# Performance work log

Hardware: AMD Instinct MI355X
Metric: run time of the kernel (lower is better)

The kernel has to match this reference:

```python
import jax, jax.numpy as jnp
import numpy as np

SCORE_WEIGHT = 0.5
MAX_ITER = 20
PROJ_ITER = 5
RELAX_LR = 0.1
EPS = 1e-8

P, D, T, O, H, W = 256, 256, 2, 24, 240, 432


def setup_inputs() -> dict:
    key = jax.random.key(0)
    k1, k2, k3, k4, k5 = jax.random.split(key, 5)
    proposed_feature = jax.random.normal(k1, (P, D), dtype=jnp.float32)
    proposed_mask = (jax.random.uniform(k2, (P, H, W)) > 0.7).astype(jnp.float32)
    template_feature = jax.random.normal(k3, (T, O, D), dtype=jnp.float32)
    mask_last_occurence = (jax.random.uniform(k4, (O, H, W)) > 0.7).astype(jnp.float32)
    proposal_score = jax.random.uniform(k5, (P,), dtype=jnp.float32)
    return {
        "proposed_feature": proposed_feature,
        "proposed_mask": proposed_mask,
        "template_feature": template_feature,
        "mask_last_occurence": mask_last_occurence,
        "proposal_score": proposal_score,
    }


def relax_matching(C, max_iter=MAX_ITER, proj_iter=PROJ_INNER if False else PROJ_ITER, lr=RELAX_LR):
    """Projected-gradient relaxation of the assignment LP.
    Gradient step on <C, X>, then proj_iter alternating projections onto
    {X >= 0, X <= 1, row sums == 1}. Returns mean of iterates (sum(X_list)/len)."""
    K, N = C.shape
    X0 = jnp.full((K, N), 1.0 / N, dtype=C.dtype)

    def project(X):
        def body(_, X):
            X = jnp.clip(X, 0.0, 1.0)
            X = X / (jnp.sum(X, axis=1, keepdims=True) + EPS)
            return X
        return jax.lax.fori_loop(0, proj_iter, body, X)

    def step(X, _):
        X = project(X - lr * C)
        return X, X

    _, Xs = jax.lax.scan(step, X0, None, length=max_iter)
    return jnp.mean(Xs, axis=0)  # [K, N]


def reference(proposed_feature, proposed_mask, template_feature,
              mask_last_occurence, proposal_score):
    n_prop = proposed_mask.shape[0]
    n_tplt = mask_last_occurence.shape[0]
    h, w = proposed_mask.shape[1], proposed_mask.shape[2]

    # --- feature cosine similarity, averaged over template frames ---
    kf = proposed_feature / (jnp.linalg.norm(proposed_feature, axis=1, keepdims=True) + EPS)
    qf = template_feature / (jnp.linalg.norm(template_feature, axis=2, keepdims=True) + EPS)
    feature_sim = jnp.einsum('tod,pd->op', qf, kf) / template_feature.shape[0]  # [O, P]

    # --- pairwise binary-mask IoU without materializing [O*P, HW] ---
    A = mask_last_occurence.reshape(n_tplt, -1)  # [O, HW] templates
    B = proposed_mask.reshape(n_prop, -1)        # [P, HW] proposals
    inter = A @ B.T                              # [O, P]
    union = A.sum(axis=1)[:, None] + B.sum(axis=1)[None, :] - inter
    iou = inter / (union + EPS)

    sim_matrix = feature_sim * (1.0 - SCORE_WEIGHT) + iou * SCORE_WEIGHT
    # P > O so no padding branch; cost is [O, P]
    cost_matrix = -sim_matrix

    Ridx = relax_matching(cost_matrix)           # averaged iterates, [O, P]
    # training branch (is_test == 0)
    logic_mask = (Ridx > 0.01).astype(Ridx.dtype)
    binX = Ridx * logic_mask

    full_outmask = (binX @ B).reshape(n_tplt, h, w)                 # [O, H, W]
    match_score = jnp.max(jnp.clip(Ridx, 0.0, 1.0) * -cost_matrix, axis=1)  # [O]
    det_score = jnp.sum(proposal_score[None, :] * binX, axis=1)     # [O]
    return (full_outmask, match_score, det_score)
```

## Files before the change

### kernel.cpp

```cpp
#include <hip/hip_runtime.h>

#define HW 103680
#define WORDS 1620
#define NGRP 405
#define NP 256
#define NO 24
#define ND 256
#define EPSF 1e-8f
#define OUTM (NO*HW)

typedef unsigned long long u64;

__device__ __forceinline__ float waveRedSum(float v) {
  v += __int_as_float(__builtin_amdgcn_update_dpp(0, __float_as_int(v), 0x111, 0xf, 0xf, false));
  v += __int_as_float(__builtin_amdgcn_update_dpp(0, __float_as_int(v), 0x112, 0xf, 0xf, false));
  v += __int_as_float(__builtin_amdgcn_update_dpp(0, __float_as_int(v), 0x114, 0xf, 0xf, false));
  v += __int_as_float(__builtin_amdgcn_update_dpp(0, __float_as_int(v), 0x118, 0xf, 0xf, false));
  v += __int_as_float(__builtin_amdgcn_update_dpp(0, __float_as_int(v), 0x142, 0xf, 0xf, false));
  v += __int_as_float(__builtin_amdgcn_update_dpp(0, __float_as_int(v), 0x143, 0xf, 0xf, false));
  return __int_as_float(__builtin_amdgcn_readlane(__float_as_int(v), 63));
}
__device__ __forceinline__ float waveMax(float v) {
#pragma unroll
  for (int m = 1; m < 64; m <<= 1) v = fmaxf(v, __shfl_xor(v, m, 64));
  return v;
}

__global__ __launch_bounds__(256) void pack_kernel(const float* __restrict__ pm,
                                                   const float* __restrict__ ml,
                                                   u64* __restrict__ bbits,
                                                   u64* __restrict__ abits,
                                                   float* __restrict__ psum) {
  int row = blockIdx.y;
  int tid = threadIdx.x, lane = tid & 63, w = tid >> 6;
  const float* rp;
  u64* bits;
  if (row < NP) { rp = pm + (size_t)row * HW;        bits = bbits + (size_t)row * WORDS; }
  else          { rp = ml + (size_t)(row - NP) * HW; bits = abits + (size_t)(row - NP) * WORDS; }
  int gid = blockIdx.x * 4 + w;
  const float* base = rp + (size_t)(gid * 6) * 256 + lane * 4;
  float4 v[6];
#pragma unroll
  for (int k = 0; k < 6; ++k) v[k] = *(const float4*)(base + k * 256);
  int cnt = 0;
#pragma unroll
  for (int k = 0; k < 6; ++k) {
    int g = gid * 6 + k;
    u64 m0 = __ballot(v[k].x != 0.0f);
    u64 m1 = __ballot(v[k].y != 0.0f);
    u64 m2 = __ballot(v[k].z != 0.0f);
    u64 m3 = __ballot(v[k].w != 0.0f);
    cnt += __popcll(m0) + __popcll(m1) + __popcll(m2) + __popcll(m3);
    if (lane == 0) {
      ulonglong2 s0; s0.x = m0; s0.y = m1;
      ulonglong2 s1; s1.x = m2; s1.y = m3;
      *(ulonglong2*)(bits + g * 4)     = s0;
      *(ulonglong2*)(bits + g * 4 + 2) = s1;
    }
  }
  if (gid < NGRP - 384) {
    int g = 384 + gid;
    float4 vv = *(const float4*)(rp + (size_t)g * 256 + lane * 4);
    u64 m0 = __ballot(vv.x != 0.0f);
    u64 m1 = __ballot(vv.y != 0.0f);
    u64 m2 = __ballot(vv.z != 0.0f);
    u64 m3 = __ballot(vv.w != 0.0f);
    cnt += __popcll(m0) + __popcll(m1) + __popcll(m2) + __popcll(m3);
    if (lane == 0) {
      ulonglong2 s0; s0.x = m0; s0.y = m1;
      ulonglong2 s1; s1.x = m2; s1.y = m3;
      *(ulonglong2*)(bits + g * 4)     = s0;
      *(ulonglong2*)(bits + g * 4 + 2) = s1;
    }
  }
  __shared__ int red[4];
  if (lane == 0) red[w] = cnt;
  __syncthreads();
  if (tid == 0) psum[row * 16 + blockIdx.x] =
      (float)((red[0] + red[1]) + (red[2] + red[3]));
}

__global__ __launch_bounds__(256) void interfeat_kernel(const u64* __restrict__ ab,
                                                        const u64* __restrict__ bb,
                                                        const float* __restrict__ pf,
                                                        const float* __restrict__ tf,
                                                        const float* __restrict__ psum,
                                                        float* __restrict__ C) {
  int wid = (blockIdx.x * 256 + threadIdx.x) >> 6;
  int lane = threadIdx.x & 63;
  int o = wid >> 8, p = wid & 255;
  const u64* ar = ab + (size_t)o * WORDS;
  const u64* br = bb + (size_t)p * WORDS;
  int cnt = 0;
  for (int w = lane; w < WORDS; w += 64)
    cnt += (int)__popcll(ar[w] & br[w]);
  float inter = waveRedSum((float)cnt);
  float4 f = *(const float4*)(pf + p * ND + lane * 4);
  float4 a = *(const float4*)(tf + o * ND + lane * 4);
  float4 b = *(const float4*)(tf + (NO + o) * ND + lane * 4);
  float nf = waveRedSum(f.x*f.x + f.y*f.y + f.z*f.z + f.w*f.w);
  float na = waveRedSum(a.x*a.x + a.y*a.y + a.z*a.z + a.w*a.w);
  float nb = waveRedSum(b.x*b.x + b.y*b.y + b.z*b.z + b.w*b.w);
  float d0 = waveRedSum(a.x*f.x + a.y*f.y + a.z*f.z + a.w*f.w);
  float d1 = waveRedSum(b.x*f.x + b.y*f.y + b.z*f.z + b.w*f.w);
  if (lane == 0) {
    float bs = 0.0f, as = 0.0f;
    const float* pb = psum + p * 16;
    const float* pa = psum + (NP + o) * 16;
#pragma unroll
    for (int q = 0; q < 16; ++q) { bs += pb[q]; as += pa[q]; }
    float invf = 1.0f / (sqrtf(nf) + EPSF);
    float inva = 1.0f / (sqrtf(na) + EPSF);
    float invb = 1.0f / (sqrtf(nb) + EPSF);
    float fs  = (d0 * inva + d1 * invb) * invf * 0.5f;
    float uni = as + bs - inter;
    float iou = inter / (uni + EPSF);
    C[wid] = -(fs * 0.5f + iou * 0.5f);
  }
}

__global__ __launch_bounds__(64) void solve_kernel(const float* __restrict__ Cm,
                                                   const float* __restrict__ score,
                                                   int* __restrict__ nzidx,
                                                   float* __restrict__ nzval,
                                                   int* __restrict__ nzcnt,
                                                   float* __restrict__ out) {
  int o = blockIdx.x, lane = threadIdx.x;
  float4 c4 = *(const float4*)(Cm + o * NP + lane * 4);
  float C[4] = {c4.x, c4.y, c4.z, c4.w};
  float sim[4], X[4], Xs[4];
#pragma unroll
  for (int j = 0; j < 4; ++j) {
    sim[j] = -C[j];
    X[j] = 1.0f / 256.0f;
    Xs[j] = 0.0f;
  }
  for (int it = 0; it < 20; ++it) {
#pragma unroll
    for (int j = 0; j < 4; ++j) X[j] = X[j] - 0.1f * C[j];
    for (int k = 0; k < 5; ++k) {
#pragma unroll
      for (int j = 0; j < 4; ++j) X[j] = fminf(fmaxf(X[j], 0.0f), 1.0f);
      float s = waveRedSum((X[0] + X[1]) + (X[2] + X[3]));
#pragma unroll
      for (int j = 0; j < 4; ++j) X[j] = X[j] / (s + EPSF);
    }
#pragma unroll
    for (int j = 0; j < 4; ++j) Xs[j] += X[j];
  }
  float R[4], bx[4];
#pragma unroll
  for (int j = 0; j < 4; ++j) {
    R[j] = Xs[j] / 20.0f;
    bx[j] = (R[j] > 0.01f) ? R[j] : 0.0f;
  }
  unsigned long long lt = (1ull << lane) - 1ull;
  int base = 0;
#pragma unroll
  for (int j = 0; j < 4; ++j) {
    unsigned long long m = __ballot(bx[j] != 0.0f);
    if (bx[j] != 0.0f) {
      int pos = base + (int)__popcll(m & lt);
      nzidx[o * NP + pos] = lane * 4 + j;
      nzval[o * NP + pos] = bx[j];
    }
    base += (int)__popcll(m);
  }
  if (lane == 0) nzcnt[o] = base;
  float mv = -1e30f;
#pragma unroll
  for (int j = 0; j < 4; ++j)
    mv = fmaxf(mv, fminf(fmaxf(R[j], 0.0f), 1.0f) * sim[j]);
  mv = waveMax(mv);
  float4 sc4 = *(const float4*)(score + lane * 4);
  float dv = waveRedSum(((sc4.x * bx[0]) + (sc4.y * bx[1])) + ((sc4.z * bx[2]) + (sc4.w * bx[3])));
  if (lane == 0) { out[OUTM + o] = mv; out[OUTM + NO + o] = dv; }
}

__global__ __launch_bounds__(256) void outmask_kernel(const float* __restrict__ pm,
                                                      const int* __restrict__ nzidx,
                                                      const float* __restrict__ nzval,
                                                      const int* __restrict__ nzcnt,
                                                      float* __restrict__ out) {
  int o = blockIdx.y;
  int t = blockIdx.x * 256 + threadIdx.x;
  int hw4 = t * 4;
  if (hw4 >= HW) return;
  int cnt = nzcnt[o];
  float4 acc = make_float4(0.0f, 0.0f, 0.0f, 0.0f);
  for (int i = 0; i < cnt; ++i) {
    int p = nzidx[o * NP + i];
    float v = nzval[o * NP + i];
    float4 m = *(const float4*)(pm + (size_t)p * HW + hw4);
    acc.x = fmaf(v, m.x, acc.x);
    acc.y = fmaf(v, m.y, acc.y);
    acc.z = fmaf(v, m.z, acc.z);
    acc.w = fmaf(v, m.w, acc.w);
  }
  *(float4*)(out + (size_t)o * HW + hw4) = acc;
}

extern "C" void kernel_launch(void* const* d_in, const int* in_sizes, int n_in,
                              void* d_out, int out_size, void* d_ws, size_t ws_size,
                              hipStream_t stream) {
  const float* pf = (const float*)d_in[0];
  const float* pm = (const float*)d_in[1];
  const float* tf = (const float*)d_in[2];
  const float* ml = (const float*)d_in[3];
  const float* sc = (const float*)d_in[4];
  float* out = (float*)d_out;
  char* ws = (char*)d_ws;

  u64*   bbits = (u64*)(ws);
  u64*   abits = (u64*)(ws + 3317760);
  int*   nzidx = (int*)(ws + 3317760);
  float* nzval = (float*)(ws + 3317760 + 24576);
  int*   nzcnt = (int*)(ws + 3317760 + 49152);
  float* Cm    = (float*)(ws + 3631136);
  float* psum  = (float*)(ws + 3680288);

  hipLaunchKernelGGL(pack_kernel,      dim3(16, 280), dim3(256), 0, stream, pm, ml, bbits, abits, psum);
  hipLaunchKernelGGL(interfeat_kernel, dim3(1536),    dim3(256), 0, stream, abits, bbits, pf, tf, psum, Cm);
  hipLaunchKernelGGL(solve_kernel,     dim3(24),      dim3(64),  0, stream, Cm, sc,
                     nzidx, nzval, nzcnt, out);
  hipLaunchKernelGGL(outmask_kernel,   dim3(102, 24), dim3(256), 0, stream, pm, nzidx, nzval, nzcnt, out);
}
```

Baseline: 57.26 us.

## Compute union via popcount of OR and drop per-row mask sum pass

The union is now counted directly as popcount(a|b) inside the intersection loop. This removes the per-block foreground counts, the shared-memory reduction in the pack kernel and the psum reads in the similarity kernel. The pack kernel changes to a grid-stride loop with 7 blocks per row instead of 16 with unrolled 6-group loads, which may cut memory-level parallelism in the bandwidth-bound pack phase. The wave max in the solve kernel now uses DPP instead of shuffles.

```diff
diff --git a/kernel.cpp b/kernel.cpp
--- a/kernel.cpp
+++ b/kernel.cpp
@@ -20,37 +20,34 @@
   v += __int_as_float(__builtin_amdgcn_update_dpp(0, __float_as_int(v), 0x143, 0xf, 0xf, false));
   return __int_as_float(__builtin_amdgcn_readlane(__float_as_int(v), 63));
 }
-__device__ __forceinline__ float waveMax(float v) {
-#pragma unroll
-  for (int m = 1; m < 64; m <<= 1) v = fmaxf(v, __shfl_xor(v, m, 64));
-  return v;
+__device__ __forceinline__ float waveRedMax(float v) {
+  int vi = __float_as_int(v);
+  v = fmaxf(v, __int_as_float(__builtin_amdgcn_update_dpp(vi, vi, 0x111, 0xf, 0xf, false))); vi = __float_as_int(v);
+  v = fmaxf(v, __int_as_float(__builtin_amdgcn_update_dpp(vi, vi, 0x112, 0xf, 0xf, false))); vi = __float_as_int(v);
+  v = fmaxf(v, __int_as_float(__builtin_amdgcn_update_dpp(vi, vi, 0x114, 0xf, 0xf, false))); vi = __float_as_int(v);
+  v = fmaxf(v, __int_as_float(__builtin_amdgcn_update_dpp(vi, vi, 0x118, 0xf, 0xf, false))); vi = __float_as_int(v);
+  v = fmaxf(v, __int_as_float(__builtin_amdgcn_update_dpp(vi, vi, 0x142, 0xf, 0xf, false))); vi = __float_as_int(v);
+  v = fmaxf(v, __int_as_float(__builtin_amdgcn_update_dpp(vi, vi, 0x143, 0xf, 0xf, false)));
+  return __int_as_float(__builtin_amdgcn_readlane(__float_as_int(v), 63));
 }
 
 __global__ __launch_bounds__(256) void pack_kernel(const float* __restrict__ pm,
                                                    const float* __restrict__ ml,
                                                    u64* __restrict__ bbits,
-                                                   u64* __restrict__ abits,
-                                                   float* __restrict__ psum) {
+                                                   u64* __restrict__ abits) {
   int row = blockIdx.y;
-  int tid = threadIdx.x, lane = tid & 63, w = tid >> 6;
+  int wir = (blockIdx.x * 256 + threadIdx.x) >> 6;
+  int lane = threadIdx.x & 63;
   const float* rp;
   u64* bits;
   if (row < NP) { rp = pm + (size_t)row * HW;        bits = bbits + (size_t)row * WORDS; }
   else          { rp = ml + (size_t)(row - NP) * HW; bits = abits + (size_t)(row - NP) * WORDS; }
-  int gid = blockIdx.x * 4 + w;
-  const float* base = rp + (size_t)(gid * 6) * 256 + lane * 4;
-  float4 v[6];
-#pragma unroll
-  for (int k = 0; k < 6; ++k) v[k] = *(const float4*)(base + k * 256);
-  int cnt = 0;
-#pragma unroll
-  for (int k = 0; k < 6; ++k) {
-    int g = gid * 6 + k;
-    u64 m0 = __ballot(v[k].x != 0.0f);
-    u64 m1 = __ballot(v[k].y != 0.0f);
-    u64 m2 = __ballot(v[k].z != 0.0f);
-    u64 m3 = __ballot(v[k].w != 0.0f);
-    cnt += __popcll(m0) + __popcll(m1) + __popcll(m2) + __popcll(m3);
+  for (int g = wir; g < NGRP; g += 28) {
+    float4 v = *(const float4*)(rp + g * 256 + lane * 4);
+    u64 m0 = __ballot(v.x != 0.0f);
+    u64 m1 = __ballot(v.y != 0.0f);
+    u64 m2 = __ballot(v.z != 0.0f);
+    u64 m3 = __ballot(v.w != 0.0f);
     if (lane == 0) {
       ulonglong2 s0; s0.x = m0; s0.y = m1;
       ulonglong2 s1; s1.x = m2; s1.y = m3;
@@ -58,43 +55,26 @@
       *(ulonglong2*)(bits + g * 4 + 2) = s1;
     }
   }
-  if (gid < NGRP - 384) {
-    int g = 384 + gid;
-    float4 vv = *(const float4*)(rp + (size_t)g * 256 + lane * 4);
-    u64 m0 = __ballot(vv.x != 0.0f);
-    u64 m1 = __ballot(vv.y != 0.0f);
-    u64 m2 = __ballot(vv.z != 0.0f);
-    u64 m3 = __ballot(vv.w != 0.0f);
-    cnt += __popcll(m0) + __popcll(m1) + __popcll(m2) + __popcll(m3);
-    if (lane == 0) {
-      ulonglong2 s0; s0.x = m0; s0.y = m1;
-      ulonglong2 s1; s1.x = m2; s1.y = m3;
-      *(ulonglong2*)(bits + g * 4)     = s0;
-      *(ulonglong2*)(bits + g * 4 + 2) = s1;
-    }
-  }
-  __shared__ int red[4];
-  if (lane == 0) red[w] = cnt;
-  __syncthreads();
-  if (tid == 0) psum[row * 16 + blockIdx.x] =
-      (float)((red[0] + red[1]) + (red[2] + red[3]));
 }
 
 __global__ __launch_bounds__(256) void interfeat_kernel(const u64* __restrict__ ab,
                                                         const u64* __restrict__ bb,
                                                         const float* __restrict__ pf,
                                                         const float* __restrict__ tf,
-                                                        const float* __restrict__ psum,
                                                         float* __restrict__ C) {
   int wid = (blockIdx.x * 256 + threadIdx.x) >> 6;
   int lane = threadIdx.x & 63;
   int o = wid >> 8, p = wid & 255;
   const u64* ar = ab + (size_t)o * WORDS;
   const u64* br = bb + (size_t)p * WORDS;
-  int cnt = 0;
-  for (int w = lane; w < WORDS; w += 64)
-    cnt += (int)__popcll(ar[w] & br[w]);
+  int cnt = 0, ucnt = 0;
+  for (int w = lane; w < WORDS; w += 64) {
+    u64 a = ar[w], b = br[w];
+    cnt  += (int)__popcll(a & b);
+    ucnt += (int)__popcll(a | b);
+  }
   float inter = waveRedSum((float)cnt);
+  float uni   = waveRedSum((float)ucnt);
   float4 f = *(const float4*)(pf + p * ND + lane * 4);
   float4 a = *(const float4*)(tf + o * ND + lane * 4);
   float4 b = *(const float4*)(tf + (NO + o) * ND + lane * 4);
@@ -104,16 +84,10 @@
   float d0 = waveRedSum(a.x*f.x + a.y*f.y + a.z*f.z + a.w*f.w);
   float d1 = waveRedSum(b.x*f.x + b.y*f.y + b.z*f.z + b.w*f.w);
   if (lane == 0) {
-    float bs = 0.0f, as = 0.0f;
-    const float* pb = psum + p * 16;
-    const float* pa = psum + (NP + o) * 16;
-#pragma unroll
-    for (int q = 0; q < 16; ++q) { bs += pb[q]; as += pa[q]; }
     float invf = 1.0f / (sqrtf(nf) + EPSF);
     float inva = 1.0f / (sqrtf(na) + EPSF);
     float invb = 1.0f / (sqrtf(nb) + EPSF);
     float fs  = (d0 * inva + d1 * invb) * invf * 0.5f;
-    float uni = as + bs - inter;
     float iou = inter / (uni + EPSF);
     C[wid] = -(fs * 0.5f + iou * 0.5f);
   }
@@ -171,7 +145,7 @@
 #pragma unroll
   for (int j = 0; j < 4; ++j)
     mv = fmaxf(mv, fminf(fmaxf(R[j], 0.0f), 1.0f) * sim[j]);
-  mv = waveMax(mv);
+  mv = waveRedMax(mv);
   float4 sc4 = *(const float4*)(score + lane * 4);
   float dv = waveRedSum(((sc4.x * bx[0]) + (sc4.y * bx[1])) + ((sc4.z * bx[2]) + (sc4.w * bx[3])));
   if (lane == 0) { out[OUTM + o] = mv; out[OUTM + NO + o] = dv; }
@@ -217,11 +191,10 @@
   float* nzval = (float*)(ws + 3317760 + 24576);
   int*   nzcnt = (int*)(ws + 3317760 + 49152);
   float* Cm    = (float*)(ws + 3631136);
-  float* psum  = (float*)(ws + 3680288);
-
-  hipLaunchKernelGGL(pack_kernel,      dim3(16, 280), dim3(256), 0, stream, pm, ml, bbits, abits, psum);
-  hipLaunchKernelGGL(interfeat_kernel, dim3(1536),    dim3(256), 0, stream, abits, bbits, pf, tf, psum, Cm);
-  hipLaunchKernelGGL(solve_kernel,     dim3(24),      dim3(64),  0, stream, Cm, sc,
+
+  hipLaunchKernelGGL(pack_kernel,      dim3(7, 280), dim3(256), 0, stream, pm, ml, bbits, abits);
+  hipLaunchKernelGGL(interfeat_kernel, dim3(1536),   dim3(256), 0, stream, abits, bbits, pf, tf, Cm);
+  hipLaunchKernelGGL(solve_kernel,     dim3(24),     dim3(64),  0, stream, Cm, sc,
                      nzidx, nzval, nzcnt, out);
   hipLaunchKernelGGL(outmask_kernel,   dim3(102, 24), dim3(256), 0, stream, pm, nzidx, nzval, nzcnt, out);
 }
```

Measured after the change: 57.19 us. About the same (-0.1%).
